# Performance work log

Hardware: AMD Instinct MI355X
Metric: run time of the kernel (lower is better)

The kernel has to match this reference:

```python
import jax, jax.numpy as jnp
import numpy as np

NUM_BINS = 256
MIN_VAL = 0.0
MAX_VAL = 1.0


def setup_inputs() -> dict:
    key = jax.random.key(0)
    images_batch = jax.random.uniform(key, (8, 3, 256, 256), dtype=jnp.float32)
    bin_centers = jnp.linspace(MIN_VAL, MAX_VAL, NUM_BINS, dtype=jnp.float32)
    return {"images_batch": images_batch, "bin_centers": bin_centers}


def reference(images_batch, bin_centers):
    # images_batch: (B, C, H, W); bin_centers: (num_bins,)
    B = images_batch.shape[0]
    num_bins = bin_centers.shape[0]
    bin_width = (MAX_VAL - MIN_VAL) / (num_bins - 1)
    images_flat = images_batch.reshape(B, -1, 1)            # (B, N, 1)
    dist = jnp.abs(images_flat - bin_centers[None, None, :])  # (B, N, num_bins)
    weights = jax.nn.relu(1.0 - dist / bin_width)
    hist = jnp.sum(weights, axis=1)                          # (B, num_bins)
    return hist
```

## Files before the change

kernel.cpp:

```cpp
#include <hip/hip_runtime.h>

#define NUM_BINS 256
#define NBATCH 8
#define N_PER_BATCH (3 * 256 * 256)
#define BLOCKS_PER_BATCH 32
#define CHUNK (N_PER_BATCH / BLOCKS_PER_BATCH)
#define THREADS 256
#define VEC_PER_THREAD (CHUNK / (THREADS * 4))

__global__ __launch_bounds__(THREADS)
void hist_partial(const float* __restrict__ img, float* __restrict__ partial) {
    __shared__ float h[4][NUM_BINS];
    const int tid  = threadIdx.x;
    const int wave = tid >> 6;

    #pragma unroll
    for (int w = 0; w < 4; ++w) h[w][tid] = 0.0f;
    __syncthreads();

    const int blk = blockIdx.x;
    const int b   = blk / BLOCKS_PER_BATCH;
    const int c   = blk % BLOCKS_PER_BATCH;
    const float4* __restrict__ src =
        (const float4*)(img + (size_t)b * N_PER_BATCH + (size_t)c * CHUNK);
    float* hw = h[wave];

    #pragma unroll
    for (int i = 0; i < VEC_PER_THREAD; ++i) {
        float4 v = src[i * THREADS + tid];
        float vals[4] = {v.x, v.y, v.z, v.w};
        #pragma unroll
        for (int j = 0; j < 4; ++j) {
            float t = vals[j] * 255.0f;
            t = fminf(fmaxf(t, 0.0f), 255.0f);
            int k = (int)t;
            if (k > 254) k = 254;
            float f = t - (float)k;
            atomicAdd(&hw[k],     1.0f - f);
            atomicAdd(&hw[k + 1], f);
        }
    }
    __syncthreads();

    float s = h[0][tid] + h[1][tid] + h[2][tid] + h[3][tid];
    partial[(size_t)blk * NUM_BINS + tid] = s;
}

__global__ __launch_bounds__(THREADS)
void hist_reduce(const float* __restrict__ partial, float* __restrict__ out) {
    const int bin = threadIdx.x;
    const int b   = blockIdx.x;
    const float* p = partial + (size_t)b * BLOCKS_PER_BATCH * NUM_BINS + bin;
    float s = 0.0f;
    #pragma unroll
    for (int c = 0; c < BLOCKS_PER_BATCH; ++c) s += p[(size_t)c * NUM_BINS];
    out[(size_t)b * NUM_BINS + bin] = s;
}

__global__ __launch_bounds__(THREADS)
void hist_atomic(const float* __restrict__ img, float* __restrict__ out) {
    __shared__ float h[4][NUM_BINS];
    const int tid  = threadIdx.x;
    const int wave = tid >> 6;
    #pragma unroll
    for (int w = 0; w < 4; ++w) h[w][tid] = 0.0f;
    __syncthreads();

    const int blk = blockIdx.x;
    const int b   = blk / BLOCKS_PER_BATCH;
    const int c   = blk % BLOCKS_PER_BATCH;
    const float4* __restrict__ src =
        (const float4*)(img + (size_t)b * N_PER_BATCH + (size_t)c * CHUNK);
    float* hw = h[wave];

    #pragma unroll
    for (int i = 0; i < VEC_PER_THREAD; ++i) {
        float4 v = src[i * THREADS + tid];
        float vals[4] = {v.x, v.y, v.z, v.w};
        #pragma unroll
        for (int j = 0; j < 4; ++j) {
            float t = vals[j] * 255.0f;
            t = fminf(fmaxf(t, 0.0f), 255.0f);
            int k = (int)t;
            if (k > 254) k = 254;
            float f = t - (float)k;
            atomicAdd(&hw[k],     1.0f - f);
            atomicAdd(&hw[k + 1], f);
        }
    }
    __syncthreads();
    float s = h[0][tid] + h[1][tid] + h[2][tid] + h[3][tid];
    atomicAdd(&out[(size_t)b * NUM_BINS + tid], s);
}

extern "C" void kernel_launch(void* const* d_in, const int* in_sizes, int n_in,
                              void* d_out, int out_size, void* d_ws, size_t ws_size,
                              hipStream_t stream) {
    const float* img = (const float*)d_in[0];
    float* out = (float*)d_out;

    const size_t ws_needed = (size_t)NBATCH * BLOCKS_PER_BATCH * NUM_BINS * sizeof(float);
    if (ws_size >= ws_needed) {
        float* partial = (float*)d_ws;
        hist_partial<<<NBATCH * BLOCKS_PER_BATCH, THREADS, 0, stream>>>(img, partial);
        hist_reduce<<<NBATCH, THREADS, 0, stream>>>(partial, out);
    } else {
        hipMemsetAsync(d_out, 0, (size_t)out_size * sizeof(float), stream);
        hist_atomic<<<NBATCH * BLOCKS_PER_BATCH, THREADS, 0, stream>>>(img, out);
    }
}
```

Baseline: 24.15 us.

## Fuse partial histogram and reduction into one cooperative kernel with grid sync

Replaces the two-kernel partial/reduce scheme with a single cooperative launch that builds per-block histograms, does a grid-wide sync, then has 64 blocks reduce the partials with a split over block groups. It also doubles the block count to 512 so each block handles a smaller chunk. The aim is to remove the second kernel launch and spread the reduction over more threads. The cost is the grid barrier, and the cooperative launch needs all 512 blocks to be co-resident.

```diff
diff --git a/kernel.cpp b/kernel.cpp
--- a/kernel.cpp
+++ b/kernel.cpp
@@ -1,16 +1,22 @@
 #include <hip/hip_runtime.h>
+#include <hip/hip_cooperative_groups.h>
+
+namespace cg = cooperative_groups;
 
 #define NUM_BINS 256
 #define NBATCH 8
 #define N_PER_BATCH (3 * 256 * 256)
-#define BLOCKS_PER_BATCH 32
+#define NBLOCKS 512
+#define BLOCKS_PER_BATCH (NBLOCKS / NBATCH)
 #define CHUNK (N_PER_BATCH / BLOCKS_PER_BATCH)
 #define THREADS 256
-#define VEC_PER_THREAD (CHUNK / (THREADS * 4))
+#define V4_PER_THREAD (CHUNK / (THREADS * 4))
 
 __global__ __launch_bounds__(THREADS)
-void hist_partial(const float* __restrict__ img, float* __restrict__ partial) {
+void hist_fused(const float* __restrict__ img, float* __restrict__ partial,
+                float* __restrict__ out) {
     __shared__ float h[4][NUM_BINS];
+    __shared__ float red[8][32];
     const int tid  = threadIdx.x;
     const int wave = tid >> 6;
 
@@ -26,7 +32,7 @@
     float* hw = h[wave];
 
     #pragma unroll
-    for (int i = 0; i < VEC_PER_THREAD; ++i) {
+    for (int i = 0; i < V4_PER_THREAD; ++i) {
         float4 v = src[i * THREADS + tid];
         float vals[4] = {v.x, v.y, v.z, v.w};
         #pragma unroll
@@ -42,19 +48,33 @@
     }
     __syncthreads();
 
-    float s = h[0][tid] + h[1][tid] + h[2][tid] + h[3][tid];
-    partial[(size_t)blk * NUM_BINS + tid] = s;
-}
+    partial[(size_t)blk * NUM_BINS + tid] =
+        h[0][tid] + h[1][tid] + h[2][tid] + h[3][tid];
 
-__global__ __launch_bounds__(THREADS)
-void hist_reduce(const float* __restrict__ partial, float* __restrict__ out) {
-    const int bin = threadIdx.x;
-    const int b   = blockIdx.x;
-    const float* p = partial + (size_t)b * BLOCKS_PER_BATCH * NUM_BINS + bin;
-    float s = 0.0f;
-    #pragma unroll
-    for (int c = 0; c < BLOCKS_PER_BATCH; ++c) s += p[(size_t)c * NUM_BINS];
-    out[(size_t)b * NUM_BINS + bin] = s;
+    cg::this_grid().sync();
+
+    if (blk < 64) {
+        const int b2  = blk >> 3;
+        const int r   = blk & 7;
+        const int bin = r * 32 + (tid & 31);
+        const int grp = tid >> 5;
+        const float* p = partial + (size_t)b2 * BLOCKS_PER_BATCH * NUM_BINS + bin;
+
+        float s = 0.0f;
+        #pragma unroll
+        for (int c2 = 0; c2 < 8; ++c2)
+            s += p[(size_t)(grp * 8 + c2) * NUM_BINS];
+
+        red[grp][tid & 31] = s;
+        __syncthreads();
+
+        if (grp == 0) {
+            float acc = 0.0f;
+            #pragma unroll
+            for (int g2 = 0; g2 < 8; ++g2) acc += red[g2][tid & 31];
+            out[(size_t)b2 * NUM_BINS + bin] = acc;
+        }
+    }
 }
 
 __global__ __launch_bounds__(THREADS)
@@ -74,7 +94,7 @@
     float* hw = h[wave];
 
     #pragma unroll
-    for (int i = 0; i < VEC_PER_THREAD; ++i) {
+    for (int i = 0; i < V4_PER_THREAD; ++i) {
         float4 v = src[i * THREADS + tid];
         float vals[4] = {v.x, v.y, v.z, v.w};
         #pragma unroll
@@ -99,13 +119,15 @@
     const float* img = (const float*)d_in[0];
     float* out = (float*)d_out;
 
-    const size_t ws_needed = (size_t)NBATCH * BLOCKS_PER_BATCH * NUM_BINS * sizeof(float);
+    const size_t ws_needed = (size_t)NBLOCKS * NUM_BINS * sizeof(float);
     if (ws_size >= ws_needed) {
         float* partial = (float*)d_ws;
-        hist_partial<<<NBATCH * BLOCKS_PER_BATCH, THREADS, 0, stream>>>(img, partial);
-        hist_reduce<<<NBATCH, THREADS, 0, stream>>>(partial, out);
+        void* args[] = { (void*)&img, (void*)&partial, (void*)&out };
+        hipLaunchCooperativeKernel((const void*)hist_fused,
+                                   dim3(NBLOCKS), dim3(THREADS),
+                                   args, 0, stream);
     } else {
         hipMemsetAsync(d_out, 0, (size_t)out_size * sizeof(float), stream);
-        hist_atomic<<<NBATCH * BLOCKS_PER_BATCH, THREADS, 0, stream>>>(img, out);
+        hist_atomic<<<NBLOCKS, THREADS, 0, stream>>>(img, out);
     }
 }
```

Result: slower. 76.70 us (+217.6%).

## Fuse partial histogram and reduction into one kernel via flag-based inter-block sync

Applied to the files above, without the earlier changes.

Replaces the two-kernel partial+reduce scheme with a single kernel. Each block publishes its partial histogram and sets a release flag. The first block of each batch spins on the batch's flags, reduces the partials and resets the flags. This removes a kernel launch and its inter-kernel gap, but relies on all blocks being co-resident and adds spin-wait latency on the reducing blocks.

```diff
diff --git a/kernel.cpp b/kernel.cpp
--- a/kernel.cpp
+++ b/kernel.cpp
@@ -4,12 +4,15 @@
 #define NBATCH 8
 #define N_PER_BATCH (3 * 256 * 256)
 #define BLOCKS_PER_BATCH 32
+#define NBLOCKS (NBATCH * BLOCKS_PER_BATCH)
 #define CHUNK (N_PER_BATCH / BLOCKS_PER_BATCH)
 #define THREADS 256
-#define VEC_PER_THREAD (CHUNK / (THREADS * 4))
+#define V4_PER_THREAD (CHUNK / (THREADS * 4))
+#define MAGIC 0x5AC0FFEEu
 
 __global__ __launch_bounds__(THREADS)
-void hist_partial(const float* __restrict__ img, float* __restrict__ partial) {
+void hist_onenode(const float* __restrict__ img, float* __restrict__ partial,
+                  unsigned* __restrict__ flags, float* __restrict__ out) {
     __shared__ float h[4][NUM_BINS];
     const int tid  = threadIdx.x;
     const int wave = tid >> 6;
@@ -26,7 +29,7 @@
     float* hw = h[wave];
 
     #pragma unroll
-    for (int i = 0; i < VEC_PER_THREAD; ++i) {
+    for (int i = 0; i < V4_PER_THREAD; ++i) {
         float4 v = src[i * THREADS + tid];
         float vals[4] = {v.x, v.y, v.z, v.w};
         #pragma unroll
@@ -42,19 +45,40 @@
     }
     __syncthreads();
 
-    float s = h[0][tid] + h[1][tid] + h[2][tid] + h[3][tid];
-    partial[(size_t)blk * NUM_BINS + tid] = s;
-}
+    partial[(size_t)blk * NUM_BINS + tid] =
+        h[0][tid] + h[1][tid] + h[2][tid] + h[3][tid];
+    __syncthreads();
+    if (tid == 0) {
+        __threadfence();
+        __hip_atomic_store(&flags[blk], MAGIC, __ATOMIC_RELEASE,
+                           __HIP_MEMORY_SCOPE_AGENT);
+    }
 
-__global__ __launch_bounds__(THREADS)
-void hist_reduce(const float* __restrict__ partial, float* __restrict__ out) {
-    const int bin = threadIdx.x;
-    const int b   = blockIdx.x;
-    const float* p = partial + (size_t)b * BLOCKS_PER_BATCH * NUM_BINS + bin;
-    float s = 0.0f;
-    #pragma unroll
-    for (int c = 0; c < BLOCKS_PER_BATCH; ++c) s += p[(size_t)c * NUM_BINS];
-    out[(size_t)b * NUM_BINS + bin] = s;
+    if (c == 0) {
+        if (tid < BLOCKS_PER_BATCH) {
+            const unsigned* fp = &flags[b * BLOCKS_PER_BATCH + tid];
+            unsigned v;
+            int guard = 0;
+            do {
+                v = __hip_atomic_load(fp, __ATOMIC_ACQUIRE,
+                                      __HIP_MEMORY_SCOPE_AGENT);
+            } while (v != MAGIC && ++guard < (1 << 24));
+        }
+        __syncthreads();
+        __threadfence();
+
+        const float* p = partial + (size_t)b * BLOCKS_PER_BATCH * NUM_BINS + tid;
+        float s = 0.0f;
+        #pragma unroll
+        for (int s2 = 0; s2 < BLOCKS_PER_BATCH; ++s2)
+            s += p[(size_t)s2 * NUM_BINS];
+        out[(size_t)b * NUM_BINS + tid] = s;
+
+        __syncthreads();
+        if (tid < BLOCKS_PER_BATCH)
+            __hip_atomic_store(&flags[b * BLOCKS_PER_BATCH + tid], 0u,
+                               __ATOMIC_RELAXED, __HIP_MEMORY_SCOPE_AGENT);
+    }
 }
 
 __global__ __launch_bounds__(THREADS)
@@ -74,7 +98,7 @@
     float* hw = h[wave];
 
     #pragma unroll
-    for (int i = 0; i < VEC_PER_THREAD; ++i) {
+    for (int i = 0; i < V4_PER_THREAD; ++i) {
         float4 v = src[i * THREADS + tid];
         float vals[4] = {v.x, v.y, v.z, v.w};
         #pragma unroll
@@ -99,13 +123,14 @@
     const float* img = (const float*)d_in[0];
     float* out = (float*)d_out;
 
-    const size_t ws_needed = (size_t)NBATCH * BLOCKS_PER_BATCH * NUM_BINS * sizeof(float);
-    if (ws_size >= ws_needed) {
-        float* partial = (float*)d_ws;
-        hist_partial<<<NBATCH * BLOCKS_PER_BATCH, THREADS, 0, stream>>>(img, partial);
-        hist_reduce<<<NBATCH, THREADS, 0, stream>>>(partial, out);
+    const size_t part_bytes = (size_t)NBLOCKS * NUM_BINS * sizeof(float);
+    const size_t flag_bytes = (size_t)NBLOCKS * sizeof(unsigned);
+    if (ws_size >= part_bytes + flag_bytes) {
+        float*    partial = (float*)d_ws;
+        unsigned* flags   = (unsigned*)((char*)d_ws + part_bytes);
+        hist_onenode<<<NBLOCKS, THREADS, 0, stream>>>(img, partial, flags, out);
     } else {
         hipMemsetAsync(d_out, 0, (size_t)out_size * sizeof(float), stream);
-        hist_atomic<<<NBATCH * BLOCKS_PER_BATCH, THREADS, 0, stream>>>(img, out);
+        hist_atomic<<<NBLOCKS, THREADS, 0, stream>>>(img, out);
     }
 }
```

Result: slower. 35.75 us (+48.0%).
